# Kernel tuning notes

Hardware: AMD Instinct MI355X
Metric: run time of the kernel (lower is better)

The kernel has to match this reference:

```python
import jax, jax.numpy as jnp
import numpy as np

B, H, NI, NT, D = 512, 1, 36, 50, 1024
NEG = -1e9
EPS = 1e-8

def setup_inputs() -> dict:
    key = jax.random.key(0)
    ks = jax.random.split(key, 12)
    s = 1.0 / np.sqrt(D)
    return {
        "imgE": jax.random.normal(ks[0], (B, H, NI, D), jnp.float32),
        "txtE": jax.random.normal(ks[1], (B, H, NT, D), jnp.float32),
        "x_mask": jax.random.randint(ks[2], (B, H, 1, NI), 0, 2).astype(bool),
        "y_mask": jax.random.randint(ks[3], (B, H, 1, NT), 0, 2).astype(bool),
        "W_img": jax.random.uniform(ks[4], (D, D), jnp.float32, -s, s),
        "b_img": jax.random.uniform(ks[5], (D,), jnp.float32, -s, s),
        "W_txt": jax.random.uniform(ks[6], (D, D), jnp.float32, -s, s),
        "b_txt": jax.random.uniform(ks[7], (D,), jnp.float32, -s, s),
        "W_img1": jax.random.uniform(ks[8], (D, D), jnp.float32, -s, s),
        "b_img1": jax.random.uniform(ks[9], (D,), jnp.float32, -s, s),
        "W_txt1": jax.random.uniform(ks[10], (D, D), jnp.float32, -s, s),
        "b_txt1": jax.random.uniform(ks[11], (D,), jnp.float32, -s, s),
    }

def reference(imgE, txtE, x_mask, y_mask,
              W_img, b_img, W_txt, b_txt, W_img1, b_img1, W_txt1, b_txt1):
    # projections
    x = jnp.einsum('bhnd,de->bhne', imgE, W_img) + b_img   # [B,H,NI,D]
    y = jnp.einsum('bhmd,de->bhme', txtE, W_txt) + b_txt   # [B,H,NT,D]
    # cosine-normalized attention scores [B,H,NI,NT]
    att = jnp.einsum('bhnd,bhmd->bhnm', x, y)
    wx = jnp.linalg.norm(x, axis=-1)[..., :, None]          # [B,H,NI,1]
    wy = jnp.linalg.norm(y, axis=-1)[..., None, :]          # [B,H,1,NT]
    att = att / jnp.maximum(wx * wy, EPS)
    # img <- txt direction
    att1 = jax.nn.softmax(jnp.where(y_mask, NEG, att), axis=-1)
    att_x = jnp.einsum('bhnm,bhmd->bhnd', att1, txtE)
    gate_x = jax.nn.sigmoid(att_x * imgE)
    fuse_x = jnp.einsum('bhnd,de->bhne', gate_x * att_x, W_img1) + b_img1
    img_out = fuse_x + imgE
    # txt <- img direction
    att2 = jax.nn.softmax(jnp.where(x_mask, NEG, jnp.swapaxes(att, 2, 3)), axis=-1)
    att_y = jnp.einsum('bhmn,bhnd->bhmd', att2, imgE)
    gate_y = jax.nn.sigmoid(att_y * txtE)
    fuse_y = jnp.einsum('bhmd,de->bhme', gate_y * att_y, W_txt1) + b_txt1
    txt_out = fuse_y + txtE
    return (img_out, txt_out)
```

## Files before the change

kernel.cpp:

```cpp
#include <hip/hip_runtime.h>

typedef unsigned short u16;
typedef unsigned int u32;
typedef __attribute__((ext_vector_type(8))) short sv8;
typedef __attribute__((ext_vector_type(4))) float fv4;

__device__ __forceinline__ u16 f2b(float f) {
  u32 u = __builtin_bit_cast(u32, f);
  u32 r = (u + 0x7fffu + ((u >> 16) & 1u)) >> 16;
  return (u16)r;
}
__device__ __forceinline__ float b2f(u16 h) {
  return __builtin_bit_cast(float, ((u32)h) << 16);
}
__device__ __forceinline__ void gld16(const void* g, void* l) {
  __builtin_amdgcn_global_load_lds(
      (const __attribute__((address_space(1))) u32*)g,
      (__attribute__((address_space(3))) u32*)l, 16, 0, 0);
}

__global__ __launch_bounds__(256) void cast_k(const float4* __restrict__ in,
                                              u16* __restrict__ out, int n4) {
  int i = blockIdx.x * 256 + threadIdx.x;
  const int stride = gridDim.x * 256;
  for (; i < n4; i += stride) {
    float4 v = in[i];
    u32 p0 = (u32)f2b(v.x) | ((u32)f2b(v.y) << 16);
    u32 p1 = (u32)f2b(v.z) | ((u32)f2b(v.w) << 16);
    uint2 o; o.x = p0; o.y = p1;
    ((uint2*)out)[i] = o;
  }
}

__global__ __launch_bounds__(256) void wtrans_k(const float* __restrict__ W0,
                                                const float* __restrict__ W1,
                                                const float* __restrict__ W2,
                                                const float* __restrict__ W3,
                                                u16* __restrict__ out) {
  const int z = blockIdx.z;
  const float* W = (z == 0) ? W0 : (z == 1) ? W1 : (z == 2) ? W2 : W3;
  u16* o = out + (size_t)z * 1048576;
  __shared__ float t[32][33];
  const int tid = threadIdx.x;
  const int r = tid >> 5, cc = tid & 31;
  const int d0 = blockIdx.x * 32, e0 = blockIdx.y * 32;
#pragma unroll
  for (int i = 0; i < 4; ++i)
    t[r + i * 8][cc] = W[(size_t)(d0 + r + i * 8) * 1024 + e0 + cc];
  __syncthreads();
#pragma unroll
  for (int i = 0; i < 4; ++i) {
    int row = r + i * 8;
    o[(size_t)(e0 + row) * 1024 + d0 + cc] = f2b(t[cc][row]);
  }
}

template <int MODE>
__global__ __launch_bounds__(512, 2) void gemm3_k(
    const u16* __restrict__ Aimg, const u16* __restrict__ Atxt,
    const u16* __restrict__ Wimg, const u16* __restrict__ Wtxt,
    const float* __restrict__ bii, const float* __restrict__ btt,
    const float* __restrict__ rii, const float* __restrict__ rtt,
    u16* __restrict__ obi, u16* __restrict__ obt,
    float* __restrict__ ofi, float* __restrict__ oft) {
  __shared__ __attribute__((aligned(16))) char smem[131072];
  const int tid = threadIdx.x;
  const int lane = tid & 63;
  const int w = tid >> 6;
  const int wm = w >> 2, wn = w & 3;
  const int l15 = lane & 15, l4 = lane >> 4;
  const int lin = blockIdx.y * 4 + blockIdx.x;
  const int xcd = lin & 7, idx = lin >> 3;
  const int s = xcd * 86 + idx;
  const int bcol0 = (s & 3) * 256;
  const int prow = s >> 2;

  const char* Ab; const char* Bb; const float* bias; const float* resid;
  u16* ob; float* of; int brow0;
  if (prow < 72) {
    brow0 = prow * 256;
    Ab = (const char*)Aimg + (size_t)brow0 * 2048;
    Bb = (const char*)Wimg + (size_t)bcol0 * 2048;
    bias = bii; resid = rii; ob = obi; of = ofi;
  } else {
    brow0 = (prow - 72) * 256;
    Ab = (const char*)Atxt + (size_t)brow0 * 2048;
    Bb = (const char*)Wtxt + (size_t)bcol0 * 2048;
    bias = btt; resid = rtt; ob = obt; of = oft;
  }

  fv4 acc[8][4] = {};
  const int srow = tid >> 3;
  const int schunk = tid & 7;

  auto STAGE = [&](int bb, int k0) {
    char* base = smem + bb * 65536;
#pragma unroll
    for (int i = 0; i < 4; ++i) {
      int row = i * 64 + srow;
      int g = schunk ^ (row & 7);
      gld16(Ab + (size_t)row * 2048 + k0 * 2 + g * 16, base + i * 8192 + tid * 16);
    }
#pragma unroll
    for (int i = 0; i < 4; ++i) {
      int row = i * 64 + srow;
      int g = schunk ^ (row & 7);
      gld16(Bb + (size_t)row * 2048 + k0 * 2 + g * 16,
            base + 32768 + i * 8192 + tid * 16);
    }
  };

  STAGE(0, 0);
  STAGE(1, 64);
  for (int t = 0; t < 16; ++t) {
    const int cur = t & 1;
    if (t < 15) asm volatile("s_waitcnt vmcnt(8)" ::: "memory");
    else        asm volatile("s_waitcnt vmcnt(0)" ::: "memory");
    __builtin_amdgcn_s_barrier();
    __builtin_amdgcn_sched_barrier(0);
    const char* Tl = smem + cur * 65536;
#pragma unroll
    for (int ks = 0; ks < 2; ++ks) {
      sv8 bf[4];
#pragma unroll
      for (int n = 0; n < 4; ++n) {
        int row = wn * 64 + n * 16 + l15;
        int c = (ks * 4 + l4) ^ (row & 7);
        bf[n] = *(const sv8*)(Tl + 32768 + row * 128 + c * 16);
      }
#pragma unroll
      for (int m = 0; m < 8; ++m) {
        int row = wm * 128 + m * 16 + l15;
        int c = (ks * 4 + l4) ^ (row & 7);
        sv8 af = *(const sv8*)(Tl + row * 128 + c * 16);
#pragma unroll
        for (int n = 0; n < 4; ++n)
          acc[m][n] = __builtin_amdgcn_mfma_f32_16x16x32_bf16(af, bf[n], acc[m][n], 0, 0, 0);
      }
    }
    __builtin_amdgcn_sched_barrier(0);
    __builtin_amdgcn_s_barrier();
    __builtin_amdgcn_sched_barrier(0);
    if (t < 14) STAGE(cur, (t + 2) * 64);
  }

#pragma unroll
  for (int n = 0; n < 4; ++n) {
    const int col = bcol0 + wn * 64 + n * 16 + l15;
    const float bv = bias[col];
#pragma unroll
    for (int m = 0; m < 8; ++m) {
      fv4 v = acc[m][n];
#pragma unroll
      for (int j = 0; j < 4; ++j) {
        const int row = brow0 + wm * 128 + m * 16 + l4 * 4 + j;
        const size_t idx2 = (size_t)row * 1024 + col;
        float r = v[j] + bv;
        if (MODE == 0) ob[idx2] = f2b(r);
        else           of[idx2] = r + resid[idx2];
      }
    }
  }
}

__global__ __launch_bounds__(512) void score_k(const u16* __restrict__ Xb,
                                               const u16* __restrict__ Yb,
                                               const void* __restrict__ xmask,
                                               const void* __restrict__ ymask,
                                               float* __restrict__ P1g,
                                               float* __restrict__ P2g) {
  __shared__ float attL[48 * 65];
  __shared__ float wxL[88];
  __shared__ unsigned char msk[88];
  const int b = blockIdx.x;
  const int tid = threadIdx.x;
  const int w = tid >> 6, lane = tid & 63;
  const int l15 = lane & 15, l4 = lane >> 4;

  u32 det = 0;
  {
    const u32* mm = (const u32*)xmask;
#pragma unroll
    for (int i = 0; i < 16; ++i) det |= mm[i * 4];
    det |= mm[1] | mm[2] | mm[3];
  }
  const bool m_i32 = (det <= 1u);
  if (tid < 36)
    msk[tid] = (unsigned char)(m_i32 ? (((const int*)xmask)[b * 36 + tid] != 0)
                                     : (((const unsigned char*)xmask)[b * 36 + tid] != 0));
  if (tid >= 64 && tid < 114) {
    int m = tid - 64;
    msk[36 + m] = (unsigned char)(m_i32 ? (((const int*)ymask)[b * 50 + m] != 0)
                                        : (((const unsigned char*)ymask)[b * 50 + m] != 0));
  }

  const u16* Xr = Xb + (size_t)b * 36864;
  const u16* Yr = Yb + (size_t)b * 51200;

  if (w < 4) {
#pragma unroll
    for (int sweep = 0; sweep < 3; ++sweep) {
      int r = sweep * 32 + (tid >> 3);
      int j = tid & 7;
      if (r < 86) {
        const u32* p = (const u32*)((r < 36) ? (Xr + r * 1024)
                                             : (Yr + (size_t)(r - 36) * 1024)) + j * 64;
        float s = 0.f;
#pragma unroll
        for (int i = 0; i < 16; ++i) {
          uint4 q = ((const uint4*)p)[i];
          u32 qq[4] = {q.x, q.y, q.z, q.w};
#pragma unroll
          for (int k2 = 0; k2 < 4; ++k2) {
            float lo = __builtin_bit_cast(float, qq[k2] << 16);
            float hi = __builtin_bit_cast(float, qq[k2] & 0xffff0000u);
            s = fmaf(lo, lo, fmaf(hi, hi, s));
          }
        }
        s += __shfl_xor(s, 1); s += __shfl_xor(s, 2); s += __shfl_xor(s, 4);
        if (j == 0) wxL[r] = sqrtf(s);
      }
    }
  } else {
    const int tn = w - 4;
    fv4 ac0 = {}, ac1 = {}, ac2 = {};
    const u16* Yp = Yr + (size_t)(tn * 16 + l15) * 1024 + l4 * 8;
    const u16* Xp = Xr + (size_t)l15 * 1024 + l4 * 8;
#pragma unroll 2
    for (int ks = 0; ks < 32; ++ks) {
      sv8 bf = *(const sv8*)(Yp + ks * 32);
      sv8 a0 = *(const sv8*)(Xp + ks * 32);
      sv8 a1 = *(const sv8*)(Xp + 16 * 1024 + ks * 32);
      sv8 a2 = *(const sv8*)(Xp + 32 * 1024 + ks * 32);
      ac0 = __builtin_amdgcn_mfma_f32_16x16x32_bf16(a0, bf, ac0, 0, 0, 0);
      ac1 = __builtin_amdgcn_mfma_f32_16x16x32_bf16(a1, bf, ac1, 0, 0, 0);
      ac2 = __builtin_amdgcn_mfma_f32_16x16x32_bf16(a2, bf, ac2, 0, 0, 0);
    }
    const int col = tn * 16 + l15;
#pragma unroll
    for (int j = 0; j < 4; ++j) {
      attL[(l4 * 4 + j) * 65 + col] = ac0[j];
      attL[(16 + l4 * 4 + j) * 65 + col] = ac1[j];
      attL[(32 + l4 * 4 + j) * 65 + col] = ac2[j];
    }
  }
  __syncthreads();

#pragma unroll
  for (int sweep = 0; sweep < 2; ++sweep) {
    int R = sweep * 64 + (tid >> 3);
    int j = tid & 7;
    if (R < 36) {
      float wxn = wxL[R];
      float sv[7];
#pragma unroll
      for (int i = 0; i < 7; ++i) {
        int m = j + i * 8;
        if (m < 50) {
          float den = fmaxf(wxn * wxL[36 + m], 1e-8f);
          float v = attL[R * 65 + m] / den;
          sv[i] = msk[36 + m] ? -1e9f : v;
        } else sv[i] = -3.4e38f;
      }
      float mx = sv[0];
#pragma unroll
      for (int i = 1; i < 7; ++i) mx = fmaxf(mx, sv[i]);
      mx = fmaxf(mx, __shfl_xor(mx, 1));
      mx = fmaxf(mx, __shfl_xor(mx, 2));
      mx = fmaxf(mx, __shfl_xor(mx, 4));
      float e[7], sum = 0.f;
#pragma unroll
      for (int i = 0; i < 7; ++i) {
        e[i] = (j + i * 8 < 50) ? __expf(sv[i] - mx) : 0.f;
        sum += e[i];
      }
      sum += __shfl_xor(sum, 1); sum += __shfl_xor(sum, 2); sum += __shfl_xor(sum, 4);
      float rs = 1.f / sum;
      float* dst = P1g + ((size_t)b * 36 + R) * 64;
#pragma unroll
      for (int i = 0; i < 7; ++i) {
        int m = j + i * 8;
        if (m < 50) dst[m] = e[i] * rs;
      }
    } else if (R < 86) {
      int m = R - 36;
      float wym = wxL[R];
      float sv[5];
#pragma unroll
      for (int i = 0; i < 5; ++i) {
        int n = j + i * 8;
        if (n < 36) {
          float den = fmaxf(wxL[n] * wym, 1e-8f);
          float v = attL[n * 65 + m] / den;
          sv[i] = msk[n] ? -1e9f : v;
        } else sv[i] = -3.4e38f;
      }
      float mx = sv[0];
#pragma unroll
      for (int i = 1; i < 5; ++i) mx = fmaxf(mx, sv[i]);
      mx = fmaxf(mx, __shfl_xor(mx, 1));
      mx = fmaxf(mx, __shfl_xor(mx, 2));
      mx = fmaxf(mx, __shfl_xor(mx, 4));
      float e[5], sum = 0.f;
#pragma unroll
      for (int i = 0; i < 5; ++i) {
        e[i] = (j + i * 8 < 36) ? __expf(sv[i] - mx) : 0.f;
        sum += e[i];
      }
      sum += __shfl_xor(sum, 1); sum += __shfl_xor(sum, 2); sum += __shfl_xor(sum, 4);
      float rs = 1.f / sum;
      float* dst = P2g + ((size_t)b * 50 + m) * 64;
#pragma unroll
      for (int i = 0; i < 5; ++i) {
        int n = j + i * 8;
        if (n < 36) dst[n] = e[i] * rs;
      }
    }
  }
}

__global__ __launch_bounds__(256) void pv_k(const float* __restrict__ P1g,
                                            const float* __restrict__ P2g,
                                            const u16* __restrict__ imgA,
                                            const u16* __restrict__ txtA,
                                            u16* __restrict__ gxw,
                                            u16* __restrict__ gyw) {
  __shared__ float ldsP1[36 * 64];
  __shared__ float ldsP2[50 * 64];
  const int b = blockIdx.x & 511;
  const int d = ((blockIdx.x >> 9) << 8) + threadIdx.x;
  const int tid = threadIdx.x;

  {
    const float4* s1 = (const float4*)(P1g + (size_t)b * 2304);
    float4* l1 = (float4*)ldsP1;
    for (int i = tid; i < 576; i += 256) l1[i] = s1[i];
    const float4* s2 = (const float4*)(P2g + (size_t)b * 3200);
    float4* l2 = (float4*)ldsP2;
    for (int i = tid; i < 800; i += 256) l2[i] = s2[i];
  }

  const u16* tp = txtA + (size_t)b * 51200 + d;
  const u16* ip = imgA + (size_t)b * 36864 + d;
  float tv[50], iv[36];
#pragma unroll
  for (int m = 0; m < 50; ++m) tv[m] = b2f(tp[(size_t)m * 1024]);
#pragma unroll
  for (int n = 0; n < 36; ++n) iv[n] = b2f(ip[(size_t)n * 1024]);
  __syncthreads();

  u16* gx = gxw + (size_t)b * 36864 + d;
#pragma unroll
  for (int n = 0; n < 36; ++n) {
    const float4* pr4 = (const float4*)(ldsP1 + n * 64);
    float4 a4 = {0.f, 0.f, 0.f, 0.f};
#pragma unroll
    for (int i = 0; i < 12; ++i) {
      float4 p = pr4[i];
      a4.x = fmaf(p.x, tv[4 * i + 0], a4.x);
      a4.y = fmaf(p.y, tv[4 * i + 1], a4.y);
      a4.z = fmaf(p.z, tv[4 * i + 2], a4.z);
      a4.w = fmaf(p.w, tv[4 * i + 3], a4.w);
    }
    float acc = (a4.x + a4.y) + (a4.z + a4.w);
    acc = fmaf(ldsP1[n * 64 + 48], tv[48], acc);
    acc = fmaf(ldsP1[n * 64 + 49], tv[49], acc);
    float t = acc * iv[n];
    float g = acc / (1.f + __expf(-t));
    gx[(size_t)n * 1024] = f2b(g);
  }
  u16* gy = gyw + (size_t)b * 51200 + d;
#pragma unroll
  for (int m = 0; m < 50; ++m) {
    const float4* pr4 = (const float4*)(ldsP2 + m * 64);
    float4 a4 = {0.f, 0.f, 0.f, 0.f};
#pragma unroll
    for (int i = 0; i < 9; ++i) {
      float4 p = pr4[i];
      a4.x = fmaf(p.x, iv[4 * i + 0], a4.x);
      a4.y = fmaf(p.y, iv[4 * i + 1], a4.y);
      a4.z = fmaf(p.z, iv[4 * i + 2], a4.z);
      a4.w = fmaf(p.w, iv[4 * i + 3], a4.w);
    }
    float acc = (a4.x + a4.y) + (a4.z + a4.w);
    float t = acc * tv[m];
    float g = acc / (1.f + __expf(-t));
    gy[(size_t)m * 1024] = f2b(g);
  }
}

extern "C" void kernel_launch(void* const* d_in, const int* in_sizes, int n_in,
                              void* d_out, int out_size, void* d_ws, size_t ws_size,
                              hipStream_t stream) {
  (void)in_sizes; (void)n_in; (void)out_size; (void)ws_size;
  const float* imgE = (const float*)d_in[0];
  const float* txtE = (const float*)d_in[1];
  const void* xmask = d_in[2];
  const void* ymask = d_in[3];
  const float* W_img  = (const float*)d_in[4];
  const float* b_img  = (const float*)d_in[5];
  const float* W_txt  = (const float*)d_in[6];
  const float* b_txt  = (const float*)d_in[7];
  const float* W_img1 = (const float*)d_in[8];
  const float* b_img1 = (const float*)d_in[9];
  const float* W_txt1 = (const float*)d_in[10];
  const float* b_txt1 = (const float*)d_in[11];
  float* out_img = (float*)d_out;
  float* out_txt = out_img + (size_t)18874368;

  char* ws = (char*)d_ws;
  u16* Wt   = (u16*)(ws);
  u16* imgA = (u16*)(ws + 8388608);
  u16* txtA = (u16*)(ws + 46137344);
  u16* Xb   = (u16*)(ws + 98566144);
  u16* Yb   = (u16*)(ws + 136314880);
  float* P1g = (float*)(ws + 188743680);
  float* P2g = (float*)(ws + 193462272);
  u16* gxw  = (u16*)(ws + 98566144);
  u16* gyw  = (u16*)(ws + 136314880);

  cast_k<<<2048, 256, 0, stream>>>((const float4*)imgE, imgA, 4718592);
  cast_k<<<2048, 256, 0, stream>>>((const float4*)txtE, txtA, 6553600);
  wtrans_k<<<dim3(32, 32, 4), 256, 0, stream>>>(W_img, W_txt, W_img1, W_txt1, Wt);
  gemm3_k<0><<<dim3(4, 172), 512, 0, stream>>>(
      imgA, txtA, Wt, Wt + 1048576, b_img, b_txt, nullptr, nullptr,
      Xb, Yb, nullptr, nullptr);
  score_k<<<512, 512, 0, stream>>>(Xb, Yb, xmask, ymask, P1g, P2g);
  pv_k<<<2048, 256, 0, stream>>>(P1g, P2g, imgA, txtA, gxw, gyw);
  gemm3_k<1><<<dim3(4, 172), 512, 0, stream>>>(
      gxw, gyw, Wt + 2097152, Wt + 3145728, b_img1, b_txt1, imgE, txtE,
      nullptr, nullptr, out_img, out_txt);
}
```

Before: 478.6 us.

## Restructure GEMM main loop into four-phase interleaved load/compute pipeline

The GEMM main loop is split into four phases per K-tile, each covering one k-substep and one half of M. Each phase issues the global-to-LDS copy for the matching slice of the next tile, then runs its MFMAs at raised wave priority. LDS slices are relaid out as 64-byte rows with a new swizzle. The aim is finer overlap of memory loads with matrix math, keeping the same double buffer. The epilogue now reads the residual and writes the output with nontemporal hints, at the cost of more barriers per tile.

```diff
diff --git a/kernel.cpp b/kernel.cpp
--- a/kernel.cpp
+++ b/kernel.cpp
@@ -56,7 +56,7 @@
 }
 
 template <int MODE>
-__global__ __launch_bounds__(512, 2) void gemm3_k(
+__global__ __launch_bounds__(512, 2) void gemm8_k(
     const u16* __restrict__ Aimg, const u16* __restrict__ Atxt,
     const u16* __restrict__ Wimg, const u16* __restrict__ Wtxt,
     const float* __restrict__ bii, const float* __restrict__ btt,
@@ -90,74 +90,98 @@
   }
 
   fv4 acc[8][4] = {};
-  const int srow = tid >> 3;
-  const int schunk = tid & 7;
-
-  auto STAGE = [&](int bb, int k0) {
-    char* base = smem + bb * 65536;
-#pragma unroll
-    for (int i = 0; i < 4; ++i) {
-      int row = i * 64 + srow;
-      int g = schunk ^ (row & 7);
-      gld16(Ab + (size_t)row * 2048 + k0 * 2 + g * 16, base + i * 8192 + tid * 16);
-    }
-#pragma unroll
-    for (int i = 0; i < 4; ++i) {
-      int row = i * 64 + srow;
-      int g = schunk ^ (row & 7);
-      gld16(Bb + (size_t)row * 2048 + k0 * 2 + g * 16,
-            base + 32768 + i * 8192 + tid * 16);
+  const int srow = tid >> 2;
+  const int schunk = tid & 3;
+
+  auto SLICE = [&](int bb, int kt, int q) {
+    const int ks = q >> 1;
+    const bool isA = (q & 1) != 0;
+    const char* src = isA ? Ab : Bb;
+    char* dst = smem + bb * 65536 + (isA ? 0 : 32768) + ks * 16384;
+#pragma unroll
+    for (int j = 0; j < 2; ++j) {
+      int row = j * 128 + srow;
+      int g = schunk ^ ((row >> 1) & 3);
+      gld16(src + (size_t)row * 2048 + kt * 128 + ks * 64 + g * 16,
+            dst + j * 8192 + tid * 16);
     }
   };
 
-  STAGE(0, 0);
-  STAGE(1, 64);
-  for (int t = 0; t < 16; ++t) {
-    const int cur = t & 1;
-    if (t < 15) asm volatile("s_waitcnt vmcnt(8)" ::: "memory");
-    else        asm volatile("s_waitcnt vmcnt(0)" ::: "memory");
-    __builtin_amdgcn_s_barrier();
-    __builtin_amdgcn_sched_barrier(0);
-    const char* Tl = smem + cur * 65536;
-#pragma unroll
-    for (int ks = 0; ks < 2; ++ks) {
-      sv8 bf[4];
+  sv8 bfr[4];
+
+#define PHASE(Rd, Q, STB, KT1, VM)                                             \
+  {                                                                            \
+    const int mh_ = (Q) & 1, ks_ = (Q) >> 1;                                   \
+    sv8 af[4];                                                                 \
+    _Pragma("unroll") for (int mi = 0; mi < 4; ++mi) {                         \
+      int r_ = wm * 128 + mh_ * 64 + mi * 16 + l15;                            \
+      af[mi] = *(const sv8*)((Rd) + ks_ * 16384 + r_ * 64 +                    \
+                             ((l4 ^ ((r_ >> 1) & 3)) * 16));                   \
+    }                                                                          \
+    if (mh_ == 0) {                                                            \
+      _Pragma("unroll") for (int n = 0; n < 4; ++n) {                          \
+        int r_ = wn * 64 + n * 16 + l15;                                       \
+        bfr[n] = *(const sv8*)((Rd) + 32768 + ks_ * 16384 + r_ * 64 +          \
+                               ((l4 ^ ((r_ >> 1) & 3)) * 16));                 \
+      }                                                                        \
+    }                                                                          \
+    if ((STB) >= 0) SLICE((STB), (KT1), (Q));                                  \
+    if ((VM) == 4) asm volatile("s_waitcnt vmcnt(4)" ::: "memory");            \
+    else asm volatile("s_waitcnt vmcnt(0)" ::: "memory");                      \
+    __builtin_amdgcn_s_barrier();                                              \
+    asm volatile("s_waitcnt lgkmcnt(0)" ::: "memory");                         \
+    __builtin_amdgcn_sched_barrier(0);                                         \
+    __builtin_amdgcn_s_setprio(1);                                             \
+    _Pragma("unroll") for (int mi = 0; mi < 4; ++mi)                           \
+      _Pragma("unroll") for (int n = 0; n < 4; ++n)                            \
+        acc[mh_ * 4 + mi][n] = __builtin_amdgcn_mfma_f32_16x16x32_bf16(        \
+            af[mi], bfr[n], acc[mh_ * 4 + mi][n], 0, 0, 0);                    \
+    __builtin_amdgcn_s_setprio(0);                                             \
+    __builtin_amdgcn_sched_barrier(0);                                         \
+    __builtin_amdgcn_s_barrier();                                              \
+  }
+
+#pragma unroll
+  for (int q = 0; q < 4; ++q) SLICE(0, 0, q);
+  asm volatile("s_waitcnt vmcnt(0)" ::: "memory");
+  __builtin_amdgcn_s_barrier();
+
+  for (int t = 0; t < 15; ++t) {
+    const char* Rd = smem + (t & 1) * 65536;
+    const int sb = (t + 1) & 1;
+    PHASE(Rd, 0, sb, t + 1, 4);
+    PHASE(Rd, 1, sb, t + 1, 4);
+    PHASE(Rd, 2, sb, t + 1, 4);
+    PHASE(Rd, 3, sb, t + 1, 4);
+  }
+  {
+    const char* Rd = smem + 65536;
+    PHASE(Rd, 0, -1, 0, 4);
+    PHASE(Rd, 1, -1, 0, 4);
+    PHASE(Rd, 2, -1, 0, 0);
+    PHASE(Rd, 3, -1, 0, 0);
+  }
+#undef PHASE
+
+  float bv[4];
+#pragma unroll
+  for (int n = 0; n < 4; ++n) bv[n] = bias[bcol0 + wn * 64 + n * 16 + l15];
+#pragma unroll
+  for (int m = 0; m < 8; ++m) {
+#pragma unroll
+    for (int j = 0; j < 4; ++j) {
+      const int row = brow0 + wm * 128 + m * 16 + l4 * 4 + j;
 #pragma unroll
       for (int n = 0; n < 4; ++n) {
-        int row = wn * 64 + n * 16 + l15;
-        int c = (ks * 4 + l4) ^ (row & 7);
-        bf[n] = *(const sv8*)(Tl + 32768 + row * 128 + c * 16);
-      }
-#pragma unroll
-      for (int m = 0; m < 8; ++m) {
-        int row = wm * 128 + m * 16 + l15;
-        int c = (ks * 4 + l4) ^ (row & 7);
-        sv8 af = *(const sv8*)(Tl + row * 128 + c * 16);
-#pragma unroll
-        for (int n = 0; n < 4; ++n)
-          acc[m][n] = __builtin_amdgcn_mfma_f32_16x16x32_bf16(af, bf[n], acc[m][n], 0, 0, 0);
-      }
-    }
-    __builtin_amdgcn_sched_barrier(0);
-    __builtin_amdgcn_s_barrier();
-    __builtin_amdgcn_sched_barrier(0);
-    if (t < 14) STAGE(cur, (t + 2) * 64);
-  }
-
-#pragma unroll
-  for (int n = 0; n < 4; ++n) {
-    const int col = bcol0 + wn * 64 + n * 16 + l15;
-    const float bv = bias[col];
-#pragma unroll
-    for (int m = 0; m < 8; ++m) {
-      fv4 v = acc[m][n];
-#pragma unroll
-      for (int j = 0; j < 4; ++j) {
-        const int row = brow0 + wm * 128 + m * 16 + l4 * 4 + j;
+        const int col = bcol0 + wn * 64 + n * 16 + l15;
         const size_t idx2 = (size_t)row * 1024 + col;
-        float r = v[j] + bv;
-        if (MODE == 0) ob[idx2] = f2b(r);
-        else           of[idx2] = r + resid[idx2];
+        float r = acc[m][n][j] + bv[n];
+        if (MODE == 0) {
+          ob[idx2] = f2b(r);
+        } else {
+          float rv = __builtin_nontemporal_load(&resid[idx2]);
+          __builtin_nontemporal_store(r + rv, &of[idx2]);
+        }
       }
     }
   }
@@ -422,12 +446,12 @@
   cast_k<<<2048, 256, 0, stream>>>((const float4*)imgE, imgA, 4718592);
   cast_k<<<2048, 256, 0, stream>>>((const float4*)txtE, txtA, 6553600);
   wtrans_k<<<dim3(32, 32, 4), 256, 0, stream>>>(W_img, W_txt, W_img1, W_txt1, Wt);
-  gemm3_k<0><<<dim3(4, 172), 512, 0, stream>>>(
+  gemm8_k<0><<<dim3(4, 172), 512, 0, stream>>>(
       imgA, txtA, Wt, Wt + 1048576, b_img, b_txt, nullptr, nullptr,
       Xb, Yb, nullptr, nullptr);
   score_k<<<512, 512, 0, stream>>>(Xb, Yb, xmask, ymask, P1g, P2g);
   pv_k<<<2048, 256, 0, stream>>>(P1g, P2g, imgA, txtA, gxw, gyw);
-  gemm3_k<1><<<dim3(4, 172), 512, 0, stream>>>(
+  gemm8_k<1><<<dim3(4, 172), 512, 0, stream>>>(
       gxw, gyw, Wt + 2097152, Wt + 3145728, b_img1, b_txt1, imgE, txtE,
       nullptr, nullptr, out_img, out_txt);
 }
```

After: 448.1 us. 6.4% less time.
